# Kernel tuning notes

Hardware: AMD Instinct MI355X
Metric: run time of the kernel (lower is better)

The kernel has to match this reference:

```python
import jax, jax.numpy as jnp
import numpy as np


def setup_inputs() -> dict:
    key = jax.random.key(0)
    ks = jax.random.split(key, 7)
    B, T, H, V = 64, 2048, 256, 256
    s = 0.05  # small init scale so tanh/sigmoid stay in a sane range
    return {
        "x": jax.random.randint(ks[0], (B, T), 0, V, dtype=jnp.int64),
        "W_ih": jax.random.normal(ks[1], (4 * H, V), dtype=jnp.float32) * s,
        "W_hh": jax.random.normal(ks[2], (4 * H, H), dtype=jnp.float32) * s,
        "b_ih": jax.random.normal(ks[3], (4 * H,), dtype=jnp.float32) * s,
        "b_hh": jax.random.normal(ks[4], (4 * H,), dtype=jnp.float32) * s,
        "fc_W": jax.random.normal(ks[5], (V, H), dtype=jnp.float32) * s,
        "fc_b": jax.random.normal(ks[6], (V,), dtype=jnp.float32) * s,
    }


def reference(x, W_ih, W_hh, b_ih, b_hh, fc_W, fc_b):
    # one_hot(x) @ W_ih.T  ==  gather rows of W_ih.T by token id (same math, no
    # [B,T,256] one-hot tensor materialized)
    B, T = x.shape
    H = W_hh.shape[1]
    x_proj = W_ih.T[x] + b_ih  # [B, T, 4H] input contributions, precomputed once

    def step(carry, xt):
        h, c = carry
        gates = xt + h @ W_hh.T + b_hh  # [B, 4H]; PyTorch gate order i,f,g,o
        i, f, g, o = jnp.split(gates, 4, axis=-1)
        i = jax.nn.sigmoid(i)
        f = jax.nn.sigmoid(f)
        g = jnp.tanh(g)
        o = jax.nn.sigmoid(o)
        c = f * c + i * g
        h = o * jnp.tanh(c)
        return (h, c), h

    h0 = jnp.zeros((B, H), dtype=x_proj.dtype)
    c0 = jnp.zeros((B, H), dtype=x_proj.dtype)
    (hT, cT), hs = jax.lax.scan(step, (h0, c0), jnp.swapaxes(x_proj, 0, 1))
    out = jnp.swapaxes(hs, 0, 1)  # [B, T, H] (batch_first)
    logits = out @ fc_W.T + fc_b  # [B, T, 256]
    return logits, hT[None], cT[None]  # h_n, c_n have shape [1, B, H]
```

## Files before the change

kernel.cpp:

```cpp
#include <hip/hip_runtime.h>
#include <stdint.h>

#define TT 2048
#define BB 64
#define HH 256

#define WIHT_OFF 0
#define BIAS_OFF 262144
#define HBUF_OFF 263168
#define XMAP_OFF 328704
#define WS_TOT   328960

#define LOGITS   33554432

__global__ __launch_bounds__(256, 1) void k_prep(const float* __restrict__ W_ih,
                                                 const float* __restrict__ b_ih,
                                                 const float* __restrict__ b_hh,
                                                 float* ws_f) {
    int idx = blockIdx.x * 256 + threadIdx.x;
    if (idx < 262144) {
        int v = idx >> 10, r = idx & 1023;
        ws_f[WIHT_OFF + idx] = W_ih[r * 256 + v];
    } else if (idx < 263168) {
        int r = idx - 262144;
        ws_f[idx] = b_ih[r] + b_hh[r];
    } else if (idx < WS_TOT) {
        ws_f[idx] = 0.0f;
    }
}

__device__ __forceinline__ float sigm_f(float x) { return 1.0f / (1.0f + __expf(-x)); }
__device__ __forceinline__ float tanh_f(float x) {
    float e = __expf(2.0f * x);
    return 1.0f - 2.0f / (e + 1.0f);
}

__device__ __forceinline__ unsigned long long ld_l2(const unsigned long long* p) {
    unsigned long long v;
    asm volatile("global_load_dwordx2 %0, %1, off sc0\n\ts_waitcnt vmcnt(0)"
                 : "=v"(v) : "v"(p) : "memory");
    return v;
}
__device__ __forceinline__ void st_l2(unsigned long long* p, unsigned long long v) {
    asm volatile("global_store_dwordx2 %0, %1, off sc0" :: "v"(p), "v"(v) : "memory");
}

__global__ __launch_bounds__(256, 1) void k_lstm(const int* __restrict__ x,
                                                 const float* __restrict__ W_hh,
                                                 const float* __restrict__ wsro,
                                                 unsigned long long* __restrict__ hbuf,
                                                 unsigned* __restrict__ xmap,
                                                 float* __restrict__ out) {
    const int tid = threadIdx.x;
    const int bid = blockIdx.x;
    const int xcd  = bid & 7;
    const int slot = bid >> 3;
    const int b = xcd + 8 * (slot >> 2);
    const int q = slot & 3;
    const int u  = tid & 63;
    const int w  = tid >> 6;
    const int j  = q * 64 + u;
    const int r  = w * 256 + j;

    __shared__ alignas(16) float hin[2][192];
    __shared__ alignas(16) float hloc[4][64];
    __shared__ float gbuf[2][256];
    __shared__ int xs[4];

    float4 w4[64];
#pragma unroll
    for (int i = 0; i < 64; ++i) {
        int cb = (i < 48) ? ((q + 1 + (i >> 4)) & 3) : q;
        int wi = (i < 48) ? (i & 15) : (i - 48);
        w4[i] = *(const float4*)(W_hh + (size_t)r * 256 + cb * 64 + wi * 4);
    }
    const float bias_r = wsro[BIAS_OFF + r];
    const int* xrow = x + b * TT;
    const bool ownw = (w == q);
    const int rb = (w - q + 3) & 3;

    int myxcc = 0;
    asm volatile("s_getreg_b32 %0, hwreg(HW_REG_XCC_ID)" : "=s"(myxcc));
    if (tid == 0)
        __hip_atomic_store(&xmap[bid], 0x100u | (unsigned)myxcc,
                           __ATOMIC_RELAXED, __HIP_MEMORY_SCOPE_AGENT);
    if (tid < 4) {
        int pb = (b & 7) + 8 * ((b >> 3) * 4 + tid);
        unsigned v; int g = 0;
        do {
            v = __hip_atomic_load(&xmap[pb], __ATOMIC_RELAXED, __HIP_MEMORY_SCOPE_AGENT);
        } while (!(v & 0x100u) && ++g < (1 << 20));
        xs[tid] = (v & 0x100u) ? (int)(v & 0xffu) : -1 - tid;
    }
    hloc[w][u] = 0.0f;
    float c_state = 0.0f;
    float hval = 0.0f;
    __syncthreads();
    bool fastm = (xs[0] == xs[1]) & (xs[1] == xs[2]) & (xs[2] == xs[3]);

    const float4* hl4 = (const float4*)hloc[w];

    float xw_cur = wsro[WIHT_OFF + xrow[0] * 1024 + r] + bias_r;

    for (int t = 0; t < TT; ++t) {
        const int p = t & 1;
        const int tn = (t + 1 < TT) ? t + 1 : t;
        const float xw_next_raw = wsro[WIHT_OFF + xrow[tn] * 1024 + r];

        float a0 = 0.f, a1 = 0.f, a2 = 0.f, a3 = 0.f;
#pragma unroll
        for (int i = 0; i < 16; ++i) {
            float4 hh = hl4[i];
            a0 += w4[48 + i].x * hh.x;
            a1 += w4[48 + i].y * hh.y;
            a2 += w4[48 + i].z * hh.z;
            a3 += w4[48 + i].w * hh.w;
        }

        if (!ownw) {
            const unsigned long long* src = hbuf + (size_t)p * (BB * HH) + b * HH + tid;
            const unsigned ut = (unsigned)t;
            unsigned long long v = 0;
            if (fastm) {
                int g = 0;
                do { v = ld_l2(src); } while ((unsigned)(v >> 32) != ut && ++g < 6000);
                if ((unsigned)(v >> 32) != ut) fastm = false;
            }
            if (!fastm) {
                int g = 0;
                do {
                    v = __hip_atomic_load(src, __ATOMIC_RELAXED, __HIP_MEMORY_SCOPE_AGENT);
                } while ((unsigned)(v >> 32) != ut && ++g < (1 << 21));
            }
            hin[p][rb * 64 + u] = __uint_as_float((unsigned)v);
        }
        __syncthreads();

        const float4* hn4 = (const float4*)hin[p];
#pragma unroll
        for (int i = 0; i < 48; ++i) {
            float4 hh = hn4[i];
            a0 += w4[i].x * hh.x;
            a1 += w4[i].y * hh.y;
            a2 += w4[i].z * hh.z;
            a3 += w4[i].w * hh.w;
        }
        float gate = xw_cur + ((a0 + a1) + (a2 + a3));
        float act = (w == 2) ? tanh_f(gate) : sigm_f(gate);
        gbuf[p][tid] = act;
        __syncthreads();

        float ig = gbuf[p][u],       fg = gbuf[p][64 + u];
        float gg = gbuf[p][128 + u], og = gbuf[p][192 + u];
        c_state = fg * c_state + ig * gg;
        hval = og * tanh_f(c_state);

        if (ownw) {
            unsigned long long pv =
                ((unsigned long long)(unsigned)(t + 1) << 32) |
                (unsigned long long)__float_as_uint(hval);
            unsigned long long* dst =
                hbuf + (size_t)((t + 1) & 1) * (BB * HH) + b * HH + j;
            if (fastm) st_l2(dst, pv);
            __hip_atomic_store(dst, pv, __ATOMIC_RELAXED, __HIP_MEMORY_SCOPE_AGENT);
            out[((size_t)(b * TT + t) << 8) + j] = hval;
        }
        hloc[w][u] = hval;
        xw_cur = xw_next_raw + bias_r;
    }

    if (ownw) {
        out[LOGITS + b * HH + j] = hval;
        out[LOGITS + BB * HH + b * HH + j] = c_state;
    }
}

__global__ __launch_bounds__(256, 1) void k_fc(const float* __restrict__ fc_W,
                                               const float* __restrict__ fc_b,
                                               float* out) {
    __shared__ alignas(16) float ht[64][256];
    const int tid = threadIdx.x;
    const size_t base = (size_t)blockIdx.x * 64;
    for (int i = 0; i < 64; ++i)
        ht[i][tid] = out[(base + i) * 256 + tid];

    float4 w4[64];
    const float4* wr = (const float4*)(fc_W + (size_t)tid * 256);
#pragma unroll
    for (int k = 0; k < 64; ++k) w4[k] = wr[k];
    const float bias = fc_b[tid];
    __syncthreads();

    for (int m = 0; m < 64; ++m) {
        const float4* hv = (const float4*)ht[m];
        float a0 = 0.f, a1 = 0.f, a2 = 0.f, a3 = 0.f;
#pragma unroll
        for (int k = 0; k < 64; ++k) {
            float4 hh = hv[k];
            a0 += w4[k].x * hh.x;
            a1 += w4[k].y * hh.y;
            a2 += w4[k].z * hh.z;
            a3 += w4[k].w * hh.w;
        }
        out[(base + m) * 256 + tid] = bias + ((a0 + a1) + (a2 + a3));
    }
}

extern "C" void kernel_launch(void* const* d_in, const int* in_sizes, int n_in,
                              void* d_out, int out_size, void* d_ws, size_t ws_size,
                              hipStream_t stream) {
    const int*   x    = (const int*)d_in[0];
    const float* W_ih = (const float*)d_in[1];
    const float* W_hh = (const float*)d_in[2];
    const float* b_ih = (const float*)d_in[3];
    const float* b_hh = (const float*)d_in[4];
    const float* fc_W = (const float*)d_in[5];
    const float* fc_b = (const float*)d_in[6];
    float* out  = (float*)d_out;
    float* ws_f = (float*)d_ws;
    unsigned long long* hbuf = (unsigned long long*)(ws_f + HBUF_OFF);
    unsigned* xmap = (unsigned*)(ws_f + XMAP_OFF);

    k_prep<<<(WS_TOT + 255) / 256, 256, 0, stream>>>(W_ih, b_ih, b_hh, ws_f);
    k_lstm<<<256, 256, 0, stream>>>(x, W_hh, ws_f, hbuf, xmap, out);
    k_fc<<<2048, 256, 0, stream>>>(fc_W, fc_b, out);
}
```

Before: 6.200 ms.

## Process two batch rows per LSTM workgroup and halve the grid

Each LSTM workgroup now advances two batch sequences (b and b+32) together, reusing the register-resident W_hh slice for both, so 128 workgroups are launched instead of 256. Cross-workgroup hidden-state polling loads both rows at once, and the token/input-projection prefetch moves one step further ahead. Barriers become raw s_barrier with an explicit LDS wait. The aim is to amortize per-step sync latency and weight reuse across two rows, at the cost of doubling serial FMA work per step on fewer CUs.

```diff
diff --git a/kernel.cpp b/kernel.cpp
--- a/kernel.cpp
+++ b/kernel.cpp
@@ -35,14 +35,24 @@
     return 1.0f - 2.0f / (e + 1.0f);
 }
 
-__device__ __forceinline__ unsigned long long ld_l2(const unsigned long long* p) {
-    unsigned long long v;
-    asm volatile("global_load_dwordx2 %0, %1, off sc0\n\ts_waitcnt vmcnt(0)"
-                 : "=v"(v) : "v"(p) : "memory");
-    return v;
+__device__ __forceinline__ void ld_l2x2(const unsigned long long* p0,
+                                        const unsigned long long* p1,
+                                        unsigned long long& v0,
+                                        unsigned long long& v1) {
+    asm volatile("global_load_dwordx2 %0, %2, off sc0\n\t"
+                 "global_load_dwordx2 %1, %3, off sc0\n\t"
+                 "s_waitcnt vmcnt(0)"
+                 : "=&v"(v0), "=&v"(v1) : "v"(p0), "v"(p1) : "memory");
 }
 __device__ __forceinline__ void st_l2(unsigned long long* p, unsigned long long v) {
     asm volatile("global_store_dwordx2 %0, %1, off sc0" :: "v"(p), "v"(v) : "memory");
+}
+
+__device__ __forceinline__ void bar_lds() {
+    asm volatile("s_waitcnt lgkmcnt(0)" ::: "memory");
+    __builtin_amdgcn_sched_barrier(0);
+    __builtin_amdgcn_s_barrier();
+    __builtin_amdgcn_sched_barrier(0);
 }
 
 __global__ __launch_bounds__(256, 1) void k_lstm(const int* __restrict__ x,
@@ -53,18 +63,20 @@
                                                  float* __restrict__ out) {
     const int tid = threadIdx.x;
     const int bid = blockIdx.x;
-    const int xcd  = bid & 7;
-    const int slot = bid >> 3;
-    const int b = xcd + 8 * (slot >> 2);
-    const int q = slot & 3;
+    const int xcd = bid & 7;
+    const int g5  = bid >> 3;
+    const int q   = g5 & 3;
+    const int pg  = g5 >> 2;
+    const int b0  = xcd + 8 * pg;
+    const int b1  = b0 + 32;
     const int u  = tid & 63;
     const int w  = tid >> 6;
     const int j  = q * 64 + u;
     const int r  = w * 256 + j;
 
-    __shared__ alignas(16) float hin[2][192];
-    __shared__ alignas(16) float hloc[4][64];
-    __shared__ float gbuf[2][256];
+    __shared__ alignas(16) float hin[2][2][192];
+    __shared__ alignas(16) float hloc[4][2][64];
+    __shared__ float gbuf[2][2][256];
     __shared__ int xs[4];
 
     float4 w4[64];
@@ -75,7 +87,8 @@
         w4[i] = *(const float4*)(W_hh + (size_t)r * 256 + cb * 64 + wi * 4);
     }
     const float bias_r = wsro[BIAS_OFF + r];
-    const int* xrow = x + b * TT;
+    const int* xrow0 = x + b0 * TT;
+    const int* xrow1 = x + b1 * TT;
     const bool ownw = (w == q);
     const int rb = (w - q + 3) & 3;
 
@@ -85,93 +98,150 @@
         __hip_atomic_store(&xmap[bid], 0x100u | (unsigned)myxcc,
                            __ATOMIC_RELAXED, __HIP_MEMORY_SCOPE_AGENT);
     if (tid < 4) {
-        int pb = (b & 7) + 8 * ((b >> 3) * 4 + tid);
+        int pb = (bid & 7) + 8 * ((pg << 2) + tid);
         unsigned v; int g = 0;
         do {
             v = __hip_atomic_load(&xmap[pb], __ATOMIC_RELAXED, __HIP_MEMORY_SCOPE_AGENT);
         } while (!(v & 0x100u) && ++g < (1 << 20));
         xs[tid] = (v & 0x100u) ? (int)(v & 0xffu) : -1 - tid;
     }
-    hloc[w][u] = 0.0f;
-    float c_state = 0.0f;
-    float hval = 0.0f;
+    hloc[w][0][u] = 0.0f;
+    hloc[w][1][u] = 0.0f;
+    float c0 = 0.0f, c1 = 0.0f;
+    float h0 = 0.0f, h1 = 0.0f;
     __syncthreads();
     bool fastm = (xs[0] == xs[1]) & (xs[1] == xs[2]) & (xs[2] == xs[3]);
 
-    const float4* hl4 = (const float4*)hloc[w];
-
-    float xw_cur = wsro[WIHT_OFF + xrow[0] * 1024 + r] + bias_r;
+    float xw0 = wsro[WIHT_OFF + xrow0[0] * 1024 + r] + bias_r;
+    float xw1 = wsro[WIHT_OFF + xrow1[0] * 1024 + r] + bias_r;
+    int tokn0 = xrow0[1], tokn1 = xrow1[1];
+
+    const float4* hl0 = (const float4*)hloc[w][0];
+    const float4* hl1 = (const float4*)hloc[w][1];
 
     for (int t = 0; t < TT; ++t) {
         const int p = t & 1;
-        const int tn = (t + 1 < TT) ? t + 1 : t;
-        const float xw_next_raw = wsro[WIHT_OFF + xrow[tn] * 1024 + r];
-
-        float a0 = 0.f, a1 = 0.f, a2 = 0.f, a3 = 0.f;
+
+        float a00 = 0.f, a01 = 0.f, a02 = 0.f, a03 = 0.f;
+        float a10 = 0.f, a11 = 0.f, a12 = 0.f, a13 = 0.f;
 #pragma unroll
         for (int i = 0; i < 16; ++i) {
-            float4 hh = hl4[i];
-            a0 += w4[48 + i].x * hh.x;
-            a1 += w4[48 + i].y * hh.y;
-            a2 += w4[48 + i].z * hh.z;
-            a3 += w4[48 + i].w * hh.w;
+            float4 hh = hl0[i];
+            a00 += w4[48 + i].x * hh.x;
+            a01 += w4[48 + i].y * hh.y;
+            a02 += w4[48 + i].z * hh.z;
+            a03 += w4[48 + i].w * hh.w;
+        }
+#pragma unroll
+        for (int i = 0; i < 16; ++i) {
+            float4 hh = hl1[i];
+            a10 += w4[48 + i].x * hh.x;
+            a11 += w4[48 + i].y * hh.y;
+            a12 += w4[48 + i].z * hh.z;
+            a13 += w4[48 + i].w * hh.w;
         }
 
         if (!ownw) {
-            const unsigned long long* src = hbuf + (size_t)p * (BB * HH) + b * HH + tid;
+            const unsigned long long* s0 =
+                hbuf + (size_t)p * (BB * HH) + b0 * HH + tid;
+            const unsigned long long* s1 =
+                hbuf + (size_t)p * (BB * HH) + b1 * HH + tid;
             const unsigned ut = (unsigned)t;
-            unsigned long long v = 0;
+            unsigned long long v0 = 0, v1 = 0;
             if (fastm) {
                 int g = 0;
-                do { v = ld_l2(src); } while ((unsigned)(v >> 32) != ut && ++g < 6000);
-                if ((unsigned)(v >> 32) != ut) fastm = false;
+                do { ld_l2x2(s0, s1, v0, v1); }
+                while (((unsigned)(v0 >> 32) != ut || (unsigned)(v1 >> 32) != ut)
+                       && ++g < 6000);
+                if ((unsigned)(v0 >> 32) != ut || (unsigned)(v1 >> 32) != ut)
+                    fastm = false;
             }
             if (!fastm) {
                 int g = 0;
                 do {
-                    v = __hip_atomic_load(src, __ATOMIC_RELAXED, __HIP_MEMORY_SCOPE_AGENT);
-                } while ((unsigned)(v >> 32) != ut && ++g < (1 << 21));
+                    if ((unsigned)(v0 >> 32) != ut)
+                        v0 = __hip_atomic_load(s0, __ATOMIC_RELAXED,
+                                               __HIP_MEMORY_SCOPE_AGENT);
+                    if ((unsigned)(v1 >> 32) != ut)
+                        v1 = __hip_atomic_load(s1, __ATOMIC_RELAXED,
+                                               __HIP_MEMORY_SCOPE_AGENT);
+                } while (((unsigned)(v0 >> 32) != ut || (unsigned)(v1 >> 32) != ut)
+                         && ++g < (1 << 21));
             }
-            hin[p][rb * 64 + u] = __uint_as_float((unsigned)v);
-        }
-        __syncthreads();
-
-        const float4* hn4 = (const float4*)hin[p];
+            hin[p][0][rb * 64 + u] = __uint_as_float((unsigned)v0);
+            hin[p][1][rb * 64 + u] = __uint_as_float((unsigned)v1);
+        }
+        bar_lds();
+
+        float xwn0 = wsro[WIHT_OFF + tokn0 * 1024 + r];
+        float xwn1 = wsro[WIHT_OFF + tokn1 * 1024 + r];
+        const int tt2 = (t + 2 < TT) ? t + 2 : TT - 1;
+        tokn0 = xrow0[tt2];
+        tokn1 = xrow1[tt2];
+
+        const float4* hn0 = (const float4*)hin[p][0];
+        const float4* hn1 = (const float4*)hin[p][1];
 #pragma unroll
         for (int i = 0; i < 48; ++i) {
-            float4 hh = hn4[i];
-            a0 += w4[i].x * hh.x;
-            a1 += w4[i].y * hh.y;
-            a2 += w4[i].z * hh.z;
-            a3 += w4[i].w * hh.w;
-        }
-        float gate = xw_cur + ((a0 + a1) + (a2 + a3));
-        float act = (w == 2) ? tanh_f(gate) : sigm_f(gate);
-        gbuf[p][tid] = act;
-        __syncthreads();
-
-        float ig = gbuf[p][u],       fg = gbuf[p][64 + u];
-        float gg = gbuf[p][128 + u], og = gbuf[p][192 + u];
-        c_state = fg * c_state + ig * gg;
-        hval = og * tanh_f(c_state);
+            float4 hh = hn0[i];
+            a00 += w4[i].x * hh.x;
+            a01 += w4[i].y * hh.y;
+            a02 += w4[i].z * hh.z;
+            a03 += w4[i].w * hh.w;
+        }
+#pragma unroll
+        for (int i = 0; i < 48; ++i) {
+            float4 hh = hn1[i];
+            a10 += w4[i].x * hh.x;
+            a11 += w4[i].y * hh.y;
+            a12 += w4[i].z * hh.z;
+            a13 += w4[i].w * hh.w;
+        }
+        float gate0 = xw0 + ((a00 + a01) + (a02 + a03));
+        float gate1 = xw1 + ((a10 + a11) + (a12 + a13));
+        float act0 = (w == 2) ? tanh_f(gate0) : sigm_f(gate0);
+        float act1 = (w == 2) ? tanh_f(gate1) : sigm_f(gate1);
+        gbuf[p][0][tid] = act0;
+        gbuf[p][1][tid] = act1;
+        bar_lds();
+
+        float i0 = gbuf[p][0][u],        f0 = gbuf[p][0][64 + u];
+        float g0 = gbuf[p][0][128 + u],  o0 = gbuf[p][0][192 + u];
+        float i1 = gbuf[p][1][u],        f1 = gbuf[p][1][64 + u];
+        float g1 = gbuf[p][1][128 + u],  o1 = gbuf[p][1][192 + u];
+        c0 = f0 * c0 + i0 * g0;
+        h0 = o0 * tanh_f(c0);
+        c1 = f1 * c1 + i1 * g1;
+        h1 = o1 * tanh_f(c1);
 
         if (ownw) {
-            unsigned long long pv =
+            unsigned long long pv0 =
                 ((unsigned long long)(unsigned)(t + 1) << 32) |
-                (unsigned long long)__float_as_uint(hval);
-            unsigned long long* dst =
-                hbuf + (size_t)((t + 1) & 1) * (BB * HH) + b * HH + j;
-            if (fastm) st_l2(dst, pv);
-            __hip_atomic_store(dst, pv, __ATOMIC_RELAXED, __HIP_MEMORY_SCOPE_AGENT);
-            out[((size_t)(b * TT + t) << 8) + j] = hval;
-        }
-        hloc[w][u] = hval;
-        xw_cur = xw_next_raw + bias_r;
+                (unsigned long long)__float_as_uint(h0);
+            unsigned long long pv1 =
+                ((unsigned long long)(unsigned)(t + 1) << 32) |
+                (unsigned long long)__float_as_uint(h1);
+            unsigned long long* d0 =
+                hbuf + (size_t)((t + 1) & 1) * (BB * HH) + b0 * HH + j;
+            unsigned long long* d1 =
+                hbuf + (size_t)((t + 1) & 1) * (BB * HH) + b1 * HH + j;
+            if (fastm) { st_l2(d0, pv0); st_l2(d1, pv1); }
+            __hip_atomic_store(d0, pv0, __ATOMIC_RELAXED, __HIP_MEMORY_SCOPE_AGENT);
+            __hip_atomic_store(d1, pv1, __ATOMIC_RELAXED, __HIP_MEMORY_SCOPE_AGENT);
+            out[((size_t)(b0 * TT + t) << 8) + j] = h0;
+            out[((size_t)(b1 * TT + t) << 8) + j] = h1;
+        }
+        hloc[w][0][u] = h0;
+        hloc[w][1][u] = h1;
+        xw0 = xwn0 + bias_r;
+        xw1 = xwn1 + bias_r;
     }
 
     if (ownw) {
-        out[LOGITS + b * HH + j] = hval;
-        out[LOGITS + BB * HH + b * HH + j] = c_state;
+        out[LOGITS + b0 * HH + j] = h0;
+        out[LOGITS + b1 * HH + j] = h1;
+        out[LOGITS + BB * HH + b0 * HH + j] = c0;
+        out[LOGITS + BB * HH + b1 * HH + j] = c1;
     }
 }
 
@@ -222,6 +292,6 @@
     unsigned* xmap = (unsigned*)(ws_f + XMAP_OFF);
 
     k_prep<<<(WS_TOT + 255) / 256, 256, 0, stream>>>(W_ih, b_ih, b_hh, ws_f);
-    k_lstm<<<256, 256, 0, stream>>>(x, W_hh, ws_f, hbuf, xmap, out);
+    k_lstm<<<128, 256, 0, stream>>>(x, W_hh, ws_f, hbuf, xmap, out);
     k_fc<<<2048, 256, 0, stream>>>(fc_W, fc_b, out);
 }
```

New measurement: 16.68 ms. 169% more time.

## Interleave gate rows per lane and exchange gates via shuffles, dropping one barrier per step

Applied to the files above, without the earlier changes.

Thread-to-row mapping changes so each group of four adjacent lanes holds the i,f,g,o gate rows of one hidden unit. The gate exchange then uses wavefront shuffles instead of an LDS buffer and a second __syncthreads per timestep. A single unified activation formula replaces the sigmoid/tanh branch. Polling is restructured so the first three waves fetch the three remote h chunks, and the XCC-detection and L2-bypass fast path are removed. This cuts per-step synchronization latency in the serial recurrence, but it may lose the faster sc0 polling path and adds shuffle traffic.

```diff
diff --git a/kernel.cpp b/kernel.cpp
--- a/kernel.cpp
+++ b/kernel.cpp
@@ -8,7 +8,6 @@
 #define WIHT_OFF 0
 #define BIAS_OFF 262144
 #define HBUF_OFF 263168
-#define XMAP_OFF 328704
 #define WS_TOT   328960
 
 #define LOGITS   33554432
@@ -29,27 +28,22 @@
     }
 }
 
-__device__ __forceinline__ float sigm_f(float x) { return 1.0f / (1.0f + __expf(-x)); }
 __device__ __forceinline__ float tanh_f(float x) {
     float e = __expf(2.0f * x);
     return 1.0f - 2.0f / (e + 1.0f);
 }
 
-__device__ __forceinline__ unsigned long long ld_l2(const unsigned long long* p) {
-    unsigned long long v;
-    asm volatile("global_load_dwordx2 %0, %1, off sc0\n\ts_waitcnt vmcnt(0)"
-                 : "=v"(v) : "v"(p) : "memory");
-    return v;
-}
-__device__ __forceinline__ void st_l2(unsigned long long* p, unsigned long long v) {
-    asm volatile("global_store_dwordx2 %0, %1, off sc0" :: "v"(p), "v"(v) : "memory");
+__device__ __forceinline__ void bar_lds() {
+    asm volatile("s_waitcnt lgkmcnt(0)" ::: "memory");
+    __builtin_amdgcn_sched_barrier(0);
+    __builtin_amdgcn_s_barrier();
+    __builtin_amdgcn_sched_barrier(0);
 }
 
 __global__ __launch_bounds__(256, 1) void k_lstm(const int* __restrict__ x,
                                                  const float* __restrict__ W_hh,
                                                  const float* __restrict__ wsro,
                                                  unsigned long long* __restrict__ hbuf,
-                                                 unsigned* __restrict__ xmap,
                                                  float* __restrict__ out) {
     const int tid = threadIdx.x;
     const int bid = blockIdx.x;
@@ -57,15 +51,14 @@
     const int slot = bid >> 3;
     const int b = xcd + 8 * (slot >> 2);
     const int q = slot & 3;
+    const int s  = tid & 3;
+    const int uj = tid >> 2;
+    const int j  = q * 64 + uj;
+    const int r  = s * 256 + j;
     const int u  = tid & 63;
-    const int w  = tid >> 6;
-    const int j  = q * 64 + u;
-    const int r  = w * 256 + j;
 
     __shared__ alignas(16) float hin[2][192];
-    __shared__ alignas(16) float hloc[4][64];
-    __shared__ float gbuf[2][256];
-    __shared__ int xs[4];
+    __shared__ alignas(16) float hloc[2][64];
 
     float4 w4[64];
 #pragma unroll
@@ -76,37 +69,41 @@
     }
     const float bias_r = wsro[BIAS_OFF + r];
     const int* xrow = x + b * TT;
-    const bool ownw = (w == q);
-    const int rb = (w - q + 3) & 3;
-
-    int myxcc = 0;
-    asm volatile("s_getreg_b32 %0, hwreg(HW_REG_XCC_ID)" : "=s"(myxcc));
-    if (tid == 0)
-        __hip_atomic_store(&xmap[bid], 0x100u | (unsigned)myxcc,
-                           __ATOMIC_RELAXED, __HIP_MEMORY_SCOPE_AGENT);
-    if (tid < 4) {
-        int pb = (b & 7) + 8 * ((b >> 3) * 4 + tid);
-        unsigned v; int g = 0;
-        do {
-            v = __hip_atomic_load(&xmap[pb], __ATOMIC_RELAXED, __HIP_MEMORY_SCOPE_AGENT);
-        } while (!(v & 0x100u) && ++g < (1 << 20));
-        xs[tid] = (v & 0x100u) ? (int)(v & 0xffu) : -1 - tid;
-    }
-    hloc[w][u] = 0.0f;
+
+    const int pk = tid >> 6;
+    const int pe = tid & 63;
+    const int cq = (q + 1 + pk) & 3;
+    const bool pollme = (tid < 192);
+
+    if (tid < 64) hloc[0][tid] = 0.0f;
     float c_state = 0.0f;
     float hval = 0.0f;
     __syncthreads();
-    bool fastm = (xs[0] == xs[1]) & (xs[1] == xs[2]) & (xs[2] == xs[3]);
-
-    const float4* hl4 = (const float4*)hloc[w];
 
     float xw_cur = wsro[WIHT_OFF + xrow[0] * 1024 + r] + bias_r;
+    int tok1 = xrow[1];
 
     for (int t = 0; t < TT; ++t) {
         const int p = t & 1;
-        const int tn = (t + 1 < TT) ? t + 1 : t;
-        const float xw_next_raw = wsro[WIHT_OFF + xrow[tn] * 1024 + r];
-
+
+        if (pollme) {
+            const unsigned long long* src =
+                hbuf + (size_t)p * (BB * HH) + b * HH + cq * 64 + pe;
+            const unsigned ut = (unsigned)t;
+            unsigned long long v = 0;
+            int g = 0;
+            do {
+                v = __hip_atomic_load(src, __ATOMIC_RELAXED, __HIP_MEMORY_SCOPE_AGENT);
+            } while ((unsigned)(v >> 32) != ut && ++g < (1 << 15));
+            hin[p][tid] = __uint_as_float((unsigned)v);
+        }
+        bar_lds();
+
+        float xw_next = wsro[WIHT_OFF + tok1 * 1024 + r];
+        tok1 = xrow[(t + 2 < TT) ? t + 2 : TT - 1];
+
+        const float4* hl4 = (const float4*)hloc[p];
+        const float4* hn4 = (const float4*)hin[p];
         float a0 = 0.f, a1 = 0.f, a2 = 0.f, a3 = 0.f;
 #pragma unroll
         for (int i = 0; i < 16; ++i) {
@@ -116,27 +113,6 @@
             a2 += w4[48 + i].z * hh.z;
             a3 += w4[48 + i].w * hh.w;
         }
-
-        if (!ownw) {
-            const unsigned long long* src = hbuf + (size_t)p * (BB * HH) + b * HH + tid;
-            const unsigned ut = (unsigned)t;
-            unsigned long long v = 0;
-            if (fastm) {
-                int g = 0;
-                do { v = ld_l2(src); } while ((unsigned)(v >> 32) != ut && ++g < 6000);
-                if ((unsigned)(v >> 32) != ut) fastm = false;
-            }
-            if (!fastm) {
-                int g = 0;
-                do {
-                    v = __hip_atomic_load(src, __ATOMIC_RELAXED, __HIP_MEMORY_SCOPE_AGENT);
-                } while ((unsigned)(v >> 32) != ut && ++g < (1 << 21));
-            }
-            hin[p][rb * 64 + u] = __uint_as_float((unsigned)v);
-        }
-        __syncthreads();
-
-        const float4* hn4 = (const float4*)hin[p];
 #pragma unroll
         for (int i = 0; i < 48; ++i) {
             float4 hh = hn4[i];
@@ -146,30 +122,35 @@
             a3 += w4[i].w * hh.w;
         }
         float gate = xw_cur + ((a0 + a1) + (a2 + a3));
-        float act = (w == 2) ? tanh_f(gate) : sigm_f(gate);
-        gbuf[p][tid] = act;
-        __syncthreads();
-
-        float ig = gbuf[p][u],       fg = gbuf[p][64 + u];
-        float gg = gbuf[p][128 + u], og = gbuf[p][192 + u];
+
+        const float B2 = (s == 2) ? 2.0f : 1.0f;
+        float ex = __expf(B2 * gate);
+        float act = 1.0f - B2 / (ex + 1.0f);
+
+        const int qb = u & ~3;
+        float ig = __shfl(act, qb + 0);
+        float fg = __shfl(act, qb + 1);
+        float gg = __shfl(act, qb + 2);
+        float og = __shfl(act, qb + 3);
         c_state = fg * c_state + ig * gg;
         hval = og * tanh_f(c_state);
 
-        if (ownw) {
+        const int pn = (t + 1) & 1;
+        if (s == 0) {
             unsigned long long pv =
                 ((unsigned long long)(unsigned)(t + 1) << 32) |
                 (unsigned long long)__float_as_uint(hval);
-            unsigned long long* dst =
-                hbuf + (size_t)((t + 1) & 1) * (BB * HH) + b * HH + j;
-            if (fastm) st_l2(dst, pv);
-            __hip_atomic_store(dst, pv, __ATOMIC_RELAXED, __HIP_MEMORY_SCOPE_AGENT);
+            __hip_atomic_store(hbuf + (size_t)pn * (BB * HH) + b * HH + j,
+                               pv, __ATOMIC_RELAXED, __HIP_MEMORY_SCOPE_AGENT);
+            hloc[pn][uj] = hval;
+        }
+        if (s == 1)
             out[((size_t)(b * TT + t) << 8) + j] = hval;
-        }
-        hloc[w][u] = hval;
-        xw_cur = xw_next_raw + bias_r;
-    }
-
-    if (ownw) {
+
+        xw_cur = xw_next + bias_r;
+    }
+
+    if (s == 0) {
         out[LOGITS + b * HH + j] = hval;
         out[LOGITS + BB * HH + b * HH + j] = c_state;
     }
@@ -219,9 +200,8 @@
     float* out  = (float*)d_out;
     float* ws_f = (float*)d_ws;
     unsigned long long* hbuf = (unsigned long long*)(ws_f + HBUF_OFF);
-    unsigned* xmap = (unsigned*)(ws_f + XMAP_OFF);
 
     k_prep<<<(WS_TOT + 255) / 256, 256, 0, stream>>>(W_ih, b_ih, b_hh, ws_f);
-    k_lstm<<<256, 256, 0, stream>>>(x, W_hh, ws_f, hbuf, xmap, out);
+    k_lstm<<<256, 256, 0, stream>>>(x, W_hh, ws_f, hbuf, out);
     k_fc<<<2048, 256, 0, stream>>>(fc_W, fc_b, out);
 }
```

After: 7.728 ms. +24.7%, slower.
